# Kernel optimization log

Measured on AMD Instinct MI355X. Metric: run time of the kernel, lower is better.

Reference implementation:

```python
import jax, jax.numpy as jnp
import numpy as np

L = 6
LVL = 2

def build_permutation_indices(L, l):
    delta = 4 ** (L - l - 1)
    tmp = np.tile(np.arange(4) * delta, delta)
    tmp += np.repeat(np.arange(delta), 4)
    tmp = np.tile(tmp, 4 ** l)
    tmp += np.repeat(np.arange(4 ** l) * 4 ** (L - l), 4 ** (L - l))
    return tmp.astype(np.int32)

def setup_inputs() -> dict:
    key = jax.random.key(0)
    ks = jax.random.split(key, 5)
    B, N, r = 16, 4 ** L, 32
    m, s = N // 4, 4 * r
    glorot = float(np.sqrt(1.0 / s))  # ~glorot scale for (s,s) matmul
    x = jax.random.normal(ks[0], (B, 2, N, r), dtype=jnp.float32)
    hr1 = jax.random.normal(ks[1], (m, s, s), dtype=jnp.float32) * glorot
    hi1 = jax.random.normal(ks[2], (m, s, s), dtype=jnp.float32) * glorot
    hr2 = jax.random.normal(ks[3], (m, s, s), dtype=jnp.float32) * glorot
    hi2 = jax.random.normal(ks[4], (m, s, s), dtype=jnp.float32) * glorot
    perm_idx = jnp.asarray(build_permutation_indices(L, LVL))
    return {"x": x, "hr1": hr1, "hi1": hi1, "hr2": hr2, "hi2": hi2, "perm_idx": perm_idx}

def reference(x, hr1, hi1, hr2, hi2, perm_idx):
    m = x.shape[-2] // 4
    s = x.shape[-1] * 4
    # permutation gather along the row axis, then regroup into m blocks of size s
    xp = jnp.take(x, perm_idx, axis=-2).reshape((-1, 2, m, s))
    x_re, x_im = xp[:, 0, :, :], xp[:, 1, :, :]
    # complex block-diagonal matmul: four real batched GEMMs over blocks 'a'
    y_re = jnp.einsum('baj,ajk->bak', x_re, hr1) + jnp.einsum('baj,ajk->bak', x_im, hi1)
    y_im = jnp.einsum('baj,ajk->bak', x_re, hi2) + jnp.einsum('baj,ajk->bak', x_im, hr2)
    y = jnp.stack([y_re, y_im], axis=1)
    n, r = m * 4, s // 4
    return y.reshape((-1, 2, n, r))
```

## Files before the change

### kernel.cpp

```cpp
#include <hip/hip_runtime.h>


__global__ __launch_bounds__(256, 4)
void hmat_kernel(const float* __restrict__ x,
                 const float* __restrict__ hr1,
                 const float* __restrict__ hi1,
                 const float* __restrict__ hr2,
                 const float* __restrict__ hi2,
                 const int* __restrict__ perm,
                 float* __restrict__ out) {
  __shared__ float x_lds[4096];
  const int a = blockIdx.x;
  const int t = threadIdx.x;

  {
    const int b    = t >> 4;
    const int c    = (t >> 3) & 1;
    const int jg   = (t >> 1) & 3;
    const int half = t & 1;
    const int row  = perm[a * 4 + jg];
    const float4* src =
        (const float4*)(x + ((size_t)(b * 2 + c) * 4096 + (size_t)row) * 32 +
                        half * 16);
#pragma unroll
    for (int q = 0; q < 4; ++q) {
      const float4 v = src[q];
      const int jb = jg * 32 + half * 16 + q * 4;
      x_lds[(jb + 0) * 32 + c * 16 + b] = v.x;
      x_lds[(jb + 1) * 32 + c * 16 + b] = v.y;
      x_lds[(jb + 2) * 32 + c * 16 + b] = v.z;
      x_lds[(jb + 3) * 32 + c * 16 + b] = v.w;
    }
  }
  __syncthreads();

  const int ch = t >> 7;
  const int u  = t & 127;
  const int bh = u >> 5;
  const int b0 = bh * 4;
  const int kg = u & 31;
  const int k0 = kg * 4;

  const float* __restrict__ H1 = (ch == 0 ? hr1 : hi2) + (size_t)a * 16384;
  const float* __restrict__ H2 = (ch == 0 ? hi1 : hr2) + (size_t)a * 16384;

  float4 acc[4];
#pragma unroll
  for (int i = 0; i < 4; ++i) acc[i] = make_float4(0.f, 0.f, 0.f, 0.f);

#pragma unroll 4
  for (int j = 0; j < 128; ++j) {
    const float4 h1 = *(const float4*)(H1 + j * 128 + k0);
    const float4 h2 = *(const float4*)(H2 + j * 128 + k0);
    const float4 xr4 = *(const float4*)&x_lds[j * 32 + b0];
    const float4 xi4 = *(const float4*)&x_lds[j * 32 + 16 + b0];
    const float xr[4] = {xr4.x, xr4.y, xr4.z, xr4.w};
    const float xi[4] = {xi4.x, xi4.y, xi4.z, xi4.w};
#pragma unroll
    for (int bb = 0; bb < 4; ++bb) {
      acc[bb].x = fmaf(xr[bb], h1.x, fmaf(xi[bb], h2.x, acc[bb].x));
      acc[bb].y = fmaf(xr[bb], h1.y, fmaf(xi[bb], h2.y, acc[bb].y));
      acc[bb].z = fmaf(xr[bb], h1.z, fmaf(xi[bb], h2.z, acc[bb].z));
      acc[bb].w = fmaf(xr[bb], h1.w, fmaf(xi[bb], h2.w, acc[bb].w));
    }
  }

#pragma unroll
  for (int bb = 0; bb < 4; ++bb) {
    const int b = b0 + bb;
    float4* dst =
        (float4*)(out + (size_t)(b * 2 + ch) * 131072 + (size_t)a * 128 + k0);
    *dst = acc[bb];
  }
}

extern "C" void kernel_launch(void* const* d_in, const int* in_sizes, int n_in,
                              void* d_out, int out_size, void* d_ws, size_t ws_size,
                              hipStream_t stream) {
  const float* x   = (const float*)d_in[0];
  const float* hr1 = (const float*)d_in[1];
  const float* hi1 = (const float*)d_in[2];
  const float* hr2 = (const float*)d_in[3];
  const float* hi2 = (const float*)d_in[4];
  const int* perm  = (const int*)d_in[5];
  float* out = (float*)d_out;

  hipLaunchKernelGGL(hmat_kernel, dim3(1024), dim3(256), 0, stream,
                     x, hr1, hi1, hr2, hi2, perm, out);
}
```

Before: 69.16 us.

## Split K across waves, hold all 16 batches per thread, prefetch H and reduce

Reorganises the per-block GEMM so each wave takes one half of the j range and each half-wave one H matrix, with every thread accumulating all 16 batch rows for four output columns. Each H element is then loaded from global exactly once per block instead of being duplicated across batch groups. H loads are software-prefetched four rows ahead. Partial sums are combined with a cross-half-wave shuffle and then an LDS reduction across the j halves. The cost is 64 accumulator registers per thread, which may lower occupancy, plus the extra reduction and synchronisation steps.

Result: faster. 57.19 us (-17.3%).

```diff
diff --git a/kernel.cpp b/kernel.cpp
--- a/kernel.cpp
+++ b/kernel.cpp
@@ -9,7 +9,7 @@
                  const float* __restrict__ hi2,
                  const int* __restrict__ perm,
                  float* __restrict__ out) {
-  __shared__ float x_lds[4096];
+  __shared__ float lds[4096];
   const int a = blockIdx.x;
   const int t = threadIdx.x;
 
@@ -26,51 +26,93 @@
     for (int q = 0; q < 4; ++q) {
       const float4 v = src[q];
       const int jb = jg * 32 + half * 16 + q * 4;
-      x_lds[(jb + 0) * 32 + c * 16 + b] = v.x;
-      x_lds[(jb + 1) * 32 + c * 16 + b] = v.y;
-      x_lds[(jb + 2) * 32 + c * 16 + b] = v.z;
-      x_lds[(jb + 3) * 32 + c * 16 + b] = v.w;
+      lds[(jb + 0) * 32 + c * 16 + b] = v.x;
+      lds[(jb + 1) * 32 + c * 16 + b] = v.y;
+      lds[(jb + 2) * 32 + c * 16 + b] = v.z;
+      lds[(jb + 3) * 32 + c * 16 + b] = v.w;
     }
   }
   __syncthreads();
 
-  const int ch = t >> 7;
-  const int u  = t & 127;
-  const int bh = u >> 5;
-  const int b0 = bh * 4;
-  const int kg = u & 31;
-  const int k0 = kg * 4;
+  const int w    = t >> 6;
+  const int ch   = w >> 1;
+  const int jh   = w & 1;
+  const int lane = t & 63;
+  const int m    = lane >> 5;
+  const int kg   = lane & 31;
+  const int k0   = kg * 4;
 
-  const float* __restrict__ H1 = (ch == 0 ? hr1 : hi2) + (size_t)a * 16384;
-  const float* __restrict__ H2 = (ch == 0 ? hi1 : hr2) + (size_t)a * 16384;
+  const float* __restrict__ Hm =
+      (ch == 0) ? (m == 0 ? hr1 : hi1) : (m == 0 ? hi2 : hr2);
+  const float* __restrict__ hp =
+      Hm + (size_t)a * 16384 + (size_t)jh * 8192 + k0;
+  const float* __restrict__ xp = lds + jh * 2048 + m * 16;
 
-  float4 acc[4];
+  float4 acc[16];
 #pragma unroll
-  for (int i = 0; i < 4; ++i) acc[i] = make_float4(0.f, 0.f, 0.f, 0.f);
+  for (int i = 0; i < 16; ++i) acc[i] = make_float4(0.f, 0.f, 0.f, 0.f);
 
-#pragma unroll 4
-  for (int j = 0; j < 128; ++j) {
-    const float4 h1 = *(const float4*)(H1 + j * 128 + k0);
-    const float4 h2 = *(const float4*)(H2 + j * 128 + k0);
-    const float4 xr4 = *(const float4*)&x_lds[j * 32 + b0];
-    const float4 xi4 = *(const float4*)&x_lds[j * 32 + 16 + b0];
-    const float xr[4] = {xr4.x, xr4.y, xr4.z, xr4.w};
-    const float xi[4] = {xi4.x, xi4.y, xi4.z, xi4.w};
-#pragma unroll
-    for (int bb = 0; bb < 4; ++bb) {
-      acc[bb].x = fmaf(xr[bb], h1.x, fmaf(xi[bb], h2.x, acc[bb].x));
-      acc[bb].y = fmaf(xr[bb], h1.y, fmaf(xi[bb], h2.y, acc[bb].y));
-      acc[bb].z = fmaf(xr[bb], h1.z, fmaf(xi[bb], h2.z, acc[bb].z));
-      acc[bb].w = fmaf(xr[bb], h1.w, fmaf(xi[bb], h2.w, acc[bb].w));
-    }
+  float4 pf0 = *(const float4*)(hp + 0 * 128);
+  float4 pf1 = *(const float4*)(hp + 1 * 128);
+  float4 pf2 = *(const float4*)(hp + 2 * 128);
+  float4 pf3 = *(const float4*)(hp + 3 * 128);
+
+#define CONSUME(PF, J)                                                     \
+  {                                                                        \
+    const float* xj = xp + (J) * 32;                                       \
+    const float4 xa = *(const float4*)(xj + 0);                            \
+    const float4 xb = *(const float4*)(xj + 4);                            \
+    const float4 xc = *(const float4*)(xj + 8);                            \
+    const float4 xd = *(const float4*)(xj + 12);                           \
+    const float xs[16] = {xa.x, xa.y, xa.z, xa.w, xb.x, xb.y, xb.z, xb.w,  \
+                          xc.x, xc.y, xc.z, xc.w, xd.x, xd.y, xd.z, xd.w}; \
+    _Pragma("unroll") for (int bb = 0; bb < 16; ++bb) {                    \
+      acc[bb].x = fmaf(xs[bb], (PF).x, acc[bb].x);                         \
+      acc[bb].y = fmaf(xs[bb], (PF).y, acc[bb].y);                         \
+      acc[bb].z = fmaf(xs[bb], (PF).z, acc[bb].z);                         \
+      acc[bb].w = fmaf(xs[bb], (PF).w, acc[bb].w);                         \
+    }                                                                      \
   }
 
+  for (int j4 = 0; j4 < 60; j4 += 4) {
+    CONSUME(pf0, j4 + 0); pf0 = *(const float4*)(hp + (j4 + 4) * 128);
+    CONSUME(pf1, j4 + 1); pf1 = *(const float4*)(hp + (j4 + 5) * 128);
+    CONSUME(pf2, j4 + 2); pf2 = *(const float4*)(hp + (j4 + 6) * 128);
+    CONSUME(pf3, j4 + 3); pf3 = *(const float4*)(hp + (j4 + 7) * 128);
+  }
+  CONSUME(pf0, 60);
+  CONSUME(pf1, 61);
+  CONSUME(pf2, 62);
+  CONSUME(pf3, 63);
+#undef CONSUME
+
 #pragma unroll
-  for (int bb = 0; bb < 4; ++bb) {
-    const int b = b0 + bb;
-    float4* dst =
-        (float4*)(out + (size_t)(b * 2 + ch) * 131072 + (size_t)a * 128 + k0);
-    *dst = acc[bb];
+  for (int bb = 0; bb < 16; ++bb) {
+    acc[bb].x += __shfl_xor(acc[bb].x, 32, 64);
+    acc[bb].y += __shfl_xor(acc[bb].y, 32, 64);
+    acc[bb].z += __shfl_xor(acc[bb].z, 32, 64);
+    acc[bb].w += __shfl_xor(acc[bb].w, 32, 64);
+  }
+
+  __syncthreads();
+  if (jh == 1 && m == 0) {
+#pragma unroll
+    for (int bb = 0; bb < 16; ++bb)
+      *(float4*)&lds[ch * 2048 + bb * 128 + k0] = acc[bb];
+  }
+  __syncthreads();
+  if (jh == 0 && m == 0) {
+#pragma unroll
+    for (int bb = 0; bb < 16; ++bb) {
+      const float4 o = *(const float4*)&lds[ch * 2048 + bb * 128 + k0];
+      float4 r;
+      r.x = acc[bb].x + o.x;
+      r.y = acc[bb].y + o.y;
+      r.z = acc[bb].z + o.z;
+      r.w = acc[bb].w + o.w;
+      *(float4*)(out + (size_t)(bb * 2 + ch) * 131072 + (size_t)a * 128 + k0) =
+          r;
+    }
   }
 }
 
```
